# Performance work log

Hardware: AMD Instinct MI355X
Metric: run time of the kernel (lower is better)

Reference implementation:

```python
import jax, jax.numpy as jnp
import numpy as np

RES = 512
NUM_COMP = 64
INIT_SCALE = 0.1
N_PTS = 1048576


def setup_inputs() -> dict:
    key = jax.random.key(0)
    k1, k2 = jax.random.split(key)
    # points in [-1, 1] as the module expects
    in_tensor = jax.random.uniform(k1, (N_PTS, 3), dtype=jnp.float32, minval=-1.0, maxval=1.0)
    plane_coef = INIT_SCALE * jax.random.normal(k2, (3, NUM_COMP, RES, RES), dtype=jnp.float32)
    return {"in_tensor": in_tensor, "plane_coef": plane_coef}


def _sample_plane(coef, xy):
    """Bilinear grid_sample, align_corners=True, padding_mode='border'.

    coef: (C, R, R) feature plane; xy: (N, 2) coords in [-1, 1], xy[:,0]->W, xy[:,1]->H.
    Returns (C, N).
    """
    C, R, _ = coef.shape
    # unnormalize (align_corners=True), then border-clamp the coordinate itself
    fx = jnp.clip((xy[:, 0] + 1.0) * 0.5 * (R - 1), 0.0, R - 1)
    fy = jnp.clip((xy[:, 1] + 1.0) * 0.5 * (R - 1), 0.0, R - 1)
    x0 = jnp.floor(fx)
    y0 = jnp.floor(fy)
    wx = fx - x0
    wy = fy - y0
    x0i = x0.astype(jnp.int32)
    y0i = y0.astype(jnp.int32)
    x1i = jnp.minimum(x0i + 1, R - 1)
    y1i = jnp.minimum(y0i + 1, R - 1)
    flat = coef.reshape(C, R * R)  # gather via flat indices: idx = y*R + x

    def g(yi, xi):
        return flat[:, yi * R + xi]  # (C, N)

    return (g(y0i, x0i) * ((1.0 - wx) * (1.0 - wy))
            + g(y0i, x1i) * (wx * (1.0 - wy))
            + g(y1i, x0i) * ((1.0 - wx) * wy)
            + g(y1i, x1i) * (wx * wy))


def reference(in_tensor, plane_coef):
    orig_shape = in_tensor.shape
    pts = in_tensor.reshape(-1, 3)
    # projections onto the xy, xz, yz planes, matching torch order
    coords = jnp.stack([pts[:, jnp.array([0, 1])],
                        pts[:, jnp.array([0, 2])],
                        pts[:, jnp.array([1, 2])]], axis=0)  # (3, N, 2)
    feats = jax.vmap(_sample_plane)(plane_coef, coords)  # (3, C, N)
    out = feats.sum(0).T  # mode == 'sum' -> (N, C)
    return out.reshape(*orig_shape[:-1], -1)
```

## Files before the change

### kernel.cpp

```cpp
#include <hip/hip_runtime.h>

#define RES   512
#define NCH   64
#define SP    (RES * RES)

#define NBITS 5
#define NSIDE (1 << NBITS)
#define NBINS (1 << (3 * NBITS))

#define TRBLK 6144

typedef float     v4f __attribute__((ext_vector_type(4)));
typedef _Float16  h4  __attribute__((ext_vector_type(4)));

__device__ __forceinline__ v4f nt_load4(const float* p)
{
    return __builtin_nontemporal_load((const v4f*)p);
}
__device__ __forceinline__ void nt_store4(float* p, v4f v)
{
    __builtin_nontemporal_store(v, (v4f*)p);
}

__device__ __forceinline__ unsigned part1by2(unsigned v)
{
    v &= 0x3FF;
    v = (v | (v << 16)) & 0x030000FF;
    v = (v | (v <<  8)) & 0x0300F00F;
    v = (v | (v <<  4)) & 0x030C30C3;
    v = (v | (v <<  2)) & 0x09249249;
    return v;
}

__device__ __forceinline__ unsigned bin_of(float x, float y, float z)
{
    int ix = (int)((x + 1.0f) * 0.5f * (float)NSIDE);
    int iy = (int)((y + 1.0f) * 0.5f * (float)NSIDE);
    int iz = (int)((z + 1.0f) * 0.5f * (float)NSIDE);
    ix = min(max(ix, 0), NSIDE - 1);
    iy = min(max(iy, 0), NSIDE - 1);
    iz = min(max(iz, 0), NSIDE - 1);
    return part1by2((unsigned)ix) | (part1by2((unsigned)iy) << 1)
         | (part1by2((unsigned)iz) << 2);
}

__global__ __launch_bounds__(256) void transpose_hist(
    const float* __restrict__ in, _Float16* __restrict__ out,
    const float* __restrict__ pts, unsigned* __restrict__ hist, int npts)
{
    __shared__ float tile[64][129];

    int b = blockIdx.x;
    if (b >= TRBLK) {
        int i = (b - TRBLK) * 256 + threadIdx.x;
        if (i < npts) {
            float x = pts[3 * (size_t)i + 0];
            float y = pts[3 * (size_t)i + 1];
            float z = pts[3 * (size_t)i + 2];
            atomicAdd(&hist[bin_of(x, y, z)], 1u);
        }
        return;
    }

    int plane = b >> 11;
    int s0    = (b & 2047) << 7;
    const float* src = in  + (size_t)plane * NCH * SP;
    _Float16*    dst = out + (size_t)plane * SP  * NCH;

    int tid = threadIdx.x;
    int r   = tid >> 4;
    int c4  = (tid & 15) << 2;

    v4f vv[8];
    #pragma unroll
    for (int it = 0; it < 8; ++it) {
        int ch = r + (it & 3) * 16;
        int sp = ((it >> 2) << 6) + c4;
        vv[it] = nt_load4(src + (size_t)ch * SP + s0 + sp);
    }
    #pragma unroll
    for (int it = 0; it < 8; ++it) {
        int ch = r + (it & 3) * 16;
        int sp = ((it >> 2) << 6) + c4;
        tile[ch][sp + 0] = vv[it][0];
        tile[ch][sp + 1] = vv[it][1];
        tile[ch][sp + 2] = vv[it][2];
        tile[ch][sp + 3] = vv[it][3];
    }
    __syncthreads();
    #pragma unroll
    for (int it = 0; it < 8; ++it) {
        int s = r + (it & 3) * 16 + ((it >> 2) << 6);
        h4 v;
        v[0] = (_Float16)tile[c4 + 0][s];
        v[1] = (_Float16)tile[c4 + 1][s];
        v[2] = (_Float16)tile[c4 + 2][s];
        v[3] = (_Float16)tile[c4 + 3][s];
        *(h4*)(dst + (size_t)(s0 + s) * NCH + c4) = v;
    }
}

__global__ __launch_bounds__(1024) void scan_kernel(
    const unsigned* __restrict__ hist, unsigned* __restrict__ offs)
{
    __shared__ unsigned partial[1024];
    int t = threadIdx.x;
    unsigned base = (unsigned)t * 32;
    unsigned local[32];
    unsigned s = 0;
    #pragma unroll
    for (int k = 0; k < 32; ++k) { local[k] = s; s += hist[base + k]; }
    partial[t] = s;
    __syncthreads();
    for (int d = 1; d < 1024; d <<= 1) {
        unsigned v = (t >= d) ? partial[t - d] : 0u;
        __syncthreads();
        partial[t] += v;
        __syncthreads();
    }
    unsigned chunk_excl = (t == 0) ? 0u : partial[t - 1];
    #pragma unroll
    for (int k = 0; k < 32; ++k) offs[base + k] = chunk_excl + local[k];
}

__global__ __launch_bounds__(256) void scatter_kernel(
    const float* __restrict__ pts, unsigned* __restrict__ offs,
    float* __restrict__ spts4, int npts)
{
    int i = blockIdx.x * 256 + threadIdx.x;
    if (i >= npts) return;
    float x = pts[3 * (size_t)i + 0];
    float y = pts[3 * (size_t)i + 1];
    float z = pts[3 * (size_t)i + 2];
    unsigned pos = atomicAdd(&offs[bin_of(x, y, z)], 1u);
    v4f v;
    v[0] = x; v[1] = y; v[2] = z; v[3] = __uint_as_float((unsigned)i);
    *(v4f*)(spts4 + 4 * (size_t)pos) = v;
}

__global__ __launch_bounds__(256) void gather_sorted(
    const float* __restrict__ spts4,
    const _Float16* __restrict__ tp, float* __restrict__ out,
    int npts, int nblk)
{
    int cpx = nblk >> 3;
    int b   = blockIdx.x;
    int swz = (b & 7) * cpx + (b >> 3);
    int t   = swz * 256 + threadIdx.x;
    int j   = t >> 4;
    if (j >= npts) return;
    int cg  = (t & 15) << 2;

    v4f s = nt_load4(spts4 + 4 * (size_t)j);
    float px = s[0], py = s[1], pz = s[2];
    unsigned idx = __float_as_uint(s[3]);

    float us[3] = {px, px, py};
    float vs[3] = {py, pz, pz};

    v4f acc = {0.f, 0.f, 0.f, 0.f};

    #pragma unroll
    for (int pl = 0; pl < 3; ++pl) {
        float fx = fminf(fmaxf((us[pl] + 1.0f) * 0.5f * 511.0f, 0.0f), 511.0f);
        float fy = fminf(fmaxf((vs[pl] + 1.0f) * 0.5f * 511.0f, 0.0f), 511.0f);
        float x0f = floorf(fx), y0f = floorf(fy);
        int   x0  = (int)x0f,  y0  = (int)y0f;
        float wx  = fx - x0f,  wy  = fy - y0f;
        int   x1  = min(x0 + 1, RES - 1);
        int   y1  = min(y0 + 1, RES - 1);

        const _Float16* base = tp + (size_t)pl * SP * NCH;
        h4 a00 = *(const h4*)(base + ((size_t)(y0 * RES + x0) * NCH) + cg);
        h4 a01 = *(const h4*)(base + ((size_t)(y0 * RES + x1) * NCH) + cg);
        h4 a10 = *(const h4*)(base + ((size_t)(y1 * RES + x0) * NCH) + cg);
        h4 a11 = *(const h4*)(base + ((size_t)(y1 * RES + x1) * NCH) + cg);

        float w00 = (1.0f - wx) * (1.0f - wy);
        float w01 = wx * (1.0f - wy);
        float w10 = (1.0f - wx) * wy;
        float w11 = wx * wy;

        v4f v00 = {(float)a00[0], (float)a00[1], (float)a00[2], (float)a00[3]};
        v4f v01 = {(float)a01[0], (float)a01[1], (float)a01[2], (float)a01[3]};
        v4f v10 = {(float)a10[0], (float)a10[1], (float)a10[2], (float)a10[3]};
        v4f v11 = {(float)a11[0], (float)a11[1], (float)a11[2], (float)a11[3]};

        acc += w00 * v00 + w01 * v01 + w10 * v10 + w11 * v11;
    }

    nt_store4(out + (size_t)idx * NCH + cg, acc);
}

__global__ __launch_bounds__(256) void gather_tp(
    const float* __restrict__ pts,
    const _Float16* __restrict__ tp,
    float* __restrict__ out, int npts)
{
    int t  = blockIdx.x * 256 + threadIdx.x;
    int pt = t >> 4;
    if (pt >= npts) return;
    int cg = (t & 15) << 2;

    float px = pts[3 * (size_t)pt + 0];
    float py = pts[3 * (size_t)pt + 1];
    float pz = pts[3 * (size_t)pt + 2];

    float us[3] = {px, px, py};
    float vs[3] = {py, pz, pz};

    v4f acc = {0.f, 0.f, 0.f, 0.f};

    #pragma unroll
    for (int pl = 0; pl < 3; ++pl) {
        float fx = fminf(fmaxf((us[pl] + 1.0f) * 0.5f * 511.0f, 0.0f), 511.0f);
        float fy = fminf(fmaxf((vs[pl] + 1.0f) * 0.5f * 511.0f, 0.0f), 511.0f);
        float x0f = floorf(fx), y0f = floorf(fy);
        int   x0  = (int)x0f,  y0  = (int)y0f;
        float wx  = fx - x0f,  wy  = fy - y0f;
        int   x1  = min(x0 + 1, RES - 1);
        int   y1  = min(y0 + 1, RES - 1);

        const _Float16* base = tp + (size_t)pl * SP * NCH;
        h4 a00 = *(const h4*)(base + ((size_t)(y0 * RES + x0) * NCH) + cg);
        h4 a01 = *(const h4*)(base + ((size_t)(y0 * RES + x1) * NCH) + cg);
        h4 a10 = *(const h4*)(base + ((size_t)(y1 * RES + x0) * NCH) + cg);
        h4 a11 = *(const h4*)(base + ((size_t)(y1 * RES + x1) * NCH) + cg);

        float w00 = (1.0f - wx) * (1.0f - wy);
        float w01 = wx * (1.0f - wy);
        float w10 = (1.0f - wx) * wy;
        float w11 = wx * wy;

        v4f v00 = {(float)a00[0], (float)a00[1], (float)a00[2], (float)a00[3]};
        v4f v01 = {(float)a01[0], (float)a01[1], (float)a01[2], (float)a01[3]};
        v4f v10 = {(float)a10[0], (float)a10[1], (float)a10[2], (float)a10[3]};
        v4f v11 = {(float)a11[0], (float)a11[1], (float)a11[2], (float)a11[3]};

        acc += w00 * v00 + w01 * v01 + w10 * v10 + w11 * v11;
    }

    *(v4f*)(out + (size_t)pt * NCH + cg) = acc;
}

__global__ __launch_bounds__(256) void gather_direct(
    const float* __restrict__ pts,
    const float* __restrict__ planes,
    float* __restrict__ out, int npts)
{
    long t = (long)blockIdx.x * 256 + threadIdx.x;
    int pt = (int)(t >> 6);
    if (pt >= npts) return;
    int ch = (int)(t & 63);

    float px = pts[3 * (size_t)pt + 0];
    float py = pts[3 * (size_t)pt + 1];
    float pz = pts[3 * (size_t)pt + 2];
    float us[3] = {px, px, py};
    float vs[3] = {py, pz, pz};

    float acc = 0.0f;
    #pragma unroll
    for (int pl = 0; pl < 3; ++pl) {
        float fx = fminf(fmaxf((us[pl] + 1.0f) * 0.5f * 511.0f, 0.0f), 511.0f);
        float fy = fminf(fmaxf((vs[pl] + 1.0f) * 0.5f * 511.0f, 0.0f), 511.0f);
        float x0f = floorf(fx), y0f = floorf(fy);
        int   x0  = (int)x0f,  y0  = (int)y0f;
        float wx  = fx - x0f,  wy  = fy - y0f;
        int   x1  = min(x0 + 1, RES - 1);
        int   y1  = min(y0 + 1, RES - 1);

        const float* base = planes + (size_t)pl * NCH * SP + (size_t)ch * SP;
        float v00 = base[y0 * RES + x0];
        float v01 = base[y0 * RES + x1];
        float v10 = base[y1 * RES + x0];
        float v11 = base[y1 * RES + x1];

        acc += v00 * ((1.0f - wx) * (1.0f - wy))
             + v01 * (wx * (1.0f - wy))
             + v10 * ((1.0f - wx) * wy)
             + v11 * (wx * wy);
    }
    out[(size_t)pt * NCH + ch] = acc;
}

extern "C" void kernel_launch(void* const* d_in, const int* in_sizes, int n_in,
                              void* d_out, int out_size, void* d_ws, size_t ws_size,
                              hipStream_t stream)
{
    (void)n_in; (void)out_size;
    const float* pts    = (const float*)d_in[0];
    const float* planes = (const float*)d_in[1];
    float*       out    = (float*)d_out;
    int npts = in_sizes[0] / 3;

    size_t sz_tp     = (size_t)3 * NCH * SP * sizeof(_Float16);
    size_t off_spts  = sz_tp;
    size_t sz_spts   = (size_t)npts * 4 * sizeof(float);
    size_t off_hist  = off_spts + sz_spts;
    size_t off_offs  = off_hist + (size_t)NBINS * sizeof(unsigned);
    size_t need_sort = off_offs + (size_t)NBINS * sizeof(unsigned);

    int nptblk = (npts + 255) / 256;

    if (ws_size >= need_sort) {
        _Float16* tp   = (_Float16*)d_ws;
        float*    sp4  = (float*)((char*)d_ws + off_spts);
        unsigned* hist = (unsigned*)((char*)d_ws + off_hist);
        unsigned* offs = (unsigned*)((char*)d_ws + off_offs);

        hipMemsetAsync(hist, 0, (size_t)NBINS * sizeof(unsigned), stream);
        transpose_hist<<<TRBLK + nptblk, 256, 0, stream>>>(
            planes, tp, pts, hist, npts);
        scan_kernel<<<1, 1024, 0, stream>>>(hist, offs);
        scatter_kernel<<<nptblk, 256, 0, stream>>>(pts, offs, sp4, npts);

        long nthr = (long)npts * 16;
        int  nblk = (int)((nthr + 255) / 256);
        nblk = (nblk + 7) & ~7;
        gather_sorted<<<nblk, 256, 0, stream>>>(sp4, tp, out, npts, nblk);
    } else if (ws_size >= sz_tp) {
        transpose_hist<<<TRBLK, 256, 0, stream>>>(
            planes, (_Float16*)d_ws, nullptr, nullptr, 0);
        long nthr = (long)npts * 16;
        gather_tp<<<(int)((nthr + 255) / 256), 256, 0, stream>>>(
            pts, (const _Float16*)d_ws, out, npts);
    } else {
        long nthr = (long)npts * 64;
        gather_direct<<<(int)((nthr + 255) / 256), 256, 0, stream>>>(
            pts, planes, out, npts);
    }
}
```

Baseline: 609.1 us.

## Fuse plane transpose with point scatter and widen gather to 8 channels

```diff
diff --git a/kernel.cpp b/kernel.cpp
--- a/kernel.cpp
+++ b/kernel.cpp
@@ -8,10 +8,11 @@
 #define NSIDE (1 << NBITS)
 #define NBINS (1 << (3 * NBITS))
 
-#define TRBLK 6144
+#define TRBLK 3072
 
 typedef float     v4f __attribute__((ext_vector_type(4)));
 typedef _Float16  h4  __attribute__((ext_vector_type(4)));
+typedef _Float16  h8  __attribute__((ext_vector_type(8)));
 
 __device__ __forceinline__ v4f nt_load4(const float* p)
 {
@@ -44,60 +45,15 @@
          | (part1by2((unsigned)iz) << 2);
 }
 
-__global__ __launch_bounds__(256) void transpose_hist(
-    const float* __restrict__ in, _Float16* __restrict__ out,
+__global__ __launch_bounds__(256) void hist_kernel(
     const float* __restrict__ pts, unsigned* __restrict__ hist, int npts)
 {
-    __shared__ float tile[64][129];
-
-    int b = blockIdx.x;
-    if (b >= TRBLK) {
-        int i = (b - TRBLK) * 256 + threadIdx.x;
-        if (i < npts) {
-            float x = pts[3 * (size_t)i + 0];
-            float y = pts[3 * (size_t)i + 1];
-            float z = pts[3 * (size_t)i + 2];
-            atomicAdd(&hist[bin_of(x, y, z)], 1u);
-        }
-        return;
-    }
-
-    int plane = b >> 11;
-    int s0    = (b & 2047) << 7;
-    const float* src = in  + (size_t)plane * NCH * SP;
-    _Float16*    dst = out + (size_t)plane * SP  * NCH;
-
-    int tid = threadIdx.x;
-    int r   = tid >> 4;
-    int c4  = (tid & 15) << 2;
-
-    v4f vv[8];
-    #pragma unroll
-    for (int it = 0; it < 8; ++it) {
-        int ch = r + (it & 3) * 16;
-        int sp = ((it >> 2) << 6) + c4;
-        vv[it] = nt_load4(src + (size_t)ch * SP + s0 + sp);
-    }
-    #pragma unroll
-    for (int it = 0; it < 8; ++it) {
-        int ch = r + (it & 3) * 16;
-        int sp = ((it >> 2) << 6) + c4;
-        tile[ch][sp + 0] = vv[it][0];
-        tile[ch][sp + 1] = vv[it][1];
-        tile[ch][sp + 2] = vv[it][2];
-        tile[ch][sp + 3] = vv[it][3];
-    }
-    __syncthreads();
-    #pragma unroll
-    for (int it = 0; it < 8; ++it) {
-        int s = r + (it & 3) * 16 + ((it >> 2) << 6);
-        h4 v;
-        v[0] = (_Float16)tile[c4 + 0][s];
-        v[1] = (_Float16)tile[c4 + 1][s];
-        v[2] = (_Float16)tile[c4 + 2][s];
-        v[3] = (_Float16)tile[c4 + 3][s];
-        *(h4*)(dst + (size_t)(s0 + s) * NCH + c4) = v;
-    }
+    int i = blockIdx.x * 256 + threadIdx.x;
+    if (i >= npts) return;
+    float x = pts[3 * (size_t)i + 0];
+    float y = pts[3 * (size_t)i + 1];
+    float z = pts[3 * (size_t)i + 2];
+    atomicAdd(&hist[bin_of(x, y, z)], 1u);
 }
 
 __global__ __launch_bounds__(1024) void scan_kernel(
@@ -123,19 +79,65 @@
     for (int k = 0; k < 32; ++k) offs[base + k] = chunk_excl + local[k];
 }
 
-__global__ __launch_bounds__(256) void scatter_kernel(
+__global__ __launch_bounds__(256) void transpose_scatter(
+    const float* __restrict__ in, _Float16* __restrict__ outp,
     const float* __restrict__ pts, unsigned* __restrict__ offs,
     float* __restrict__ spts4, int npts)
 {
-    int i = blockIdx.x * 256 + threadIdx.x;
-    if (i >= npts) return;
-    float x = pts[3 * (size_t)i + 0];
-    float y = pts[3 * (size_t)i + 1];
-    float z = pts[3 * (size_t)i + 2];
-    unsigned pos = atomicAdd(&offs[bin_of(x, y, z)], 1u);
-    v4f v;
-    v[0] = x; v[1] = y; v[2] = z; v[3] = __uint_as_float((unsigned)i);
-    *(v4f*)(spts4 + 4 * (size_t)pos) = v;
+    __shared__ _Float16 tile[256][72];
+
+    int b    = blockIdx.x;
+    int id   = b >> 1;
+    if ((b & 1) == 0) {
+        if (pts == nullptr) return;
+        int i = id * 256 + threadIdx.x;
+        if (i < npts) {
+            float x = pts[3 * (size_t)i + 0];
+            float y = pts[3 * (size_t)i + 1];
+            float z = pts[3 * (size_t)i + 2];
+            unsigned pos = atomicAdd(&offs[bin_of(x, y, z)], 1u);
+            v4f v;
+            v[0] = x; v[1] = y; v[2] = z; v[3] = __uint_as_float((unsigned)i);
+            *(v4f*)(spts4 + 4 * (size_t)pos) = v;
+        }
+        return;
+    }
+    if (id >= TRBLK) return;
+
+    int plane = id >> 10;
+    int s0    = (id & 1023) << 8;
+    const float* src = in   + (size_t)plane * NCH * SP;
+    _Float16*    dst = outp + (size_t)plane * SP  * NCH;
+
+    int w = threadIdx.x >> 6;
+    int l = threadIdx.x & 63;
+
+    #pragma unroll
+    for (int g = 0; g < 4; ++g) {
+        int c0 = w * 16 + g * 4;
+        v4f v0 = nt_load4(src + (size_t)(c0 + 0) * SP + s0 + 4 * l);
+        v4f v1 = nt_load4(src + (size_t)(c0 + 1) * SP + s0 + 4 * l);
+        v4f v2 = nt_load4(src + (size_t)(c0 + 2) * SP + s0 + 4 * l);
+        v4f v3 = nt_load4(src + (size_t)(c0 + 3) * SP + s0 + 4 * l);
+        #pragma unroll
+        for (int i = 0; i < 4; ++i) {
+            h4 hv;
+            hv[0] = (_Float16)v0[i];
+            hv[1] = (_Float16)v1[i];
+            hv[2] = (_Float16)v2[i];
+            hv[3] = (_Float16)v3[i];
+            *(h4*)&tile[4 * l + i][c0] = hv;
+        }
+    }
+    __syncthreads();
+
+    #pragma unroll
+    for (int j = 0; j < 8; ++j) {
+        int texel = w * 64 + j * 8 + (l >> 3);
+        int oct   = (l & 7) << 3;
+        h8 hv = *(const h8*)&tile[texel][oct];
+        *(h8*)(dst + (size_t)(s0 + texel) * NCH + oct) = hv;
+    }
 }
 
 __global__ __launch_bounds__(256) void gather_sorted(
@@ -147,9 +149,9 @@
     int b   = blockIdx.x;
     int swz = (b & 7) * cpx + (b >> 3);
     int t   = swz * 256 + threadIdx.x;
-    int j   = t >> 4;
+    int j   = t >> 3;
     if (j >= npts) return;
-    int cg  = (t & 15) << 2;
+    int cg  = (t & 7) << 3;
 
     v4f s = nt_load4(spts4 + 4 * (size_t)j);
     float px = s[0], py = s[1], pz = s[2];
@@ -158,7 +160,8 @@
     float us[3] = {px, px, py};
     float vs[3] = {py, pz, pz};
 
-    v4f acc = {0.f, 0.f, 0.f, 0.f};
+    v4f acc0 = {0.f, 0.f, 0.f, 0.f};
+    v4f acc1 = {0.f, 0.f, 0.f, 0.f};
 
     #pragma unroll
     for (int pl = 0; pl < 3; ++pl) {
@@ -171,25 +174,27 @@
         int   y1  = min(y0 + 1, RES - 1);
 
         const _Float16* base = tp + (size_t)pl * SP * NCH;
-        h4 a00 = *(const h4*)(base + ((size_t)(y0 * RES + x0) * NCH) + cg);
-        h4 a01 = *(const h4*)(base + ((size_t)(y0 * RES + x1) * NCH) + cg);
-        h4 a10 = *(const h4*)(base + ((size_t)(y1 * RES + x0) * NCH) + cg);
-        h4 a11 = *(const h4*)(base + ((size_t)(y1 * RES + x1) * NCH) + cg);
+        h8 a00 = *(const h8*)(base + ((size_t)(y0 * RES + x0) * NCH) + cg);
+        h8 a01 = *(const h8*)(base + ((size_t)(y0 * RES + x1) * NCH) + cg);
+        h8 a10 = *(const h8*)(base + ((size_t)(y1 * RES + x0) * NCH) + cg);
+        h8 a11 = *(const h8*)(base + ((size_t)(y1 * RES + x1) * NCH) + cg);
 
         float w00 = (1.0f - wx) * (1.0f - wy);
         float w01 = wx * (1.0f - wy);
         float w10 = (1.0f - wx) * wy;
         float w11 = wx * wy;
 
-        v4f v00 = {(float)a00[0], (float)a00[1], (float)a00[2], (float)a00[3]};
-        v4f v01 = {(float)a01[0], (float)a01[1], (float)a01[2], (float)a01[3]};
-        v4f v10 = {(float)a10[0], (float)a10[1], (float)a10[2], (float)a10[3]};
-        v4f v11 = {(float)a11[0], (float)a11[1], (float)a11[2], (float)a11[3]};
-
-        acc += w00 * v00 + w01 * v01 + w10 * v10 + w11 * v11;
-    }
-
-    nt_store4(out + (size_t)idx * NCH + cg, acc);
+        #pragma unroll
+        for (int k = 0; k < 4; ++k) {
+            acc0[k] += w00 * (float)a00[k] + w01 * (float)a01[k]
+                     + w10 * (float)a10[k] + w11 * (float)a11[k];
+            acc1[k] += w00 * (float)a00[k + 4] + w01 * (float)a01[k + 4]
+                     + w10 * (float)a10[k + 4] + w11 * (float)a11[k + 4];
+        }
+    }
+
+    nt_store4(out + (size_t)idx * NCH + cg,     acc0);
+    nt_store4(out + (size_t)idx * NCH + cg + 4, acc1);
 }
 
 __global__ __launch_bounds__(256) void gather_tp(
@@ -198,9 +203,9 @@
     float* __restrict__ out, int npts)
 {
     int t  = blockIdx.x * 256 + threadIdx.x;
-    int pt = t >> 4;
+    int pt = t >> 3;
     if (pt >= npts) return;
-    int cg = (t & 15) << 2;
+    int cg = (t & 7) << 3;
 
     float px = pts[3 * (size_t)pt + 0];
     float py = pts[3 * (size_t)pt + 1];
@@ -209,7 +214,8 @@
     float us[3] = {px, px, py};
     float vs[3] = {py, pz, pz};
 
-    v4f acc = {0.f, 0.f, 0.f, 0.f};
+    v4f acc0 = {0.f, 0.f, 0.f, 0.f};
+    v4f acc1 = {0.f, 0.f, 0.f, 0.f};
 
     #pragma unroll
     for (int pl = 0; pl < 3; ++pl) {
@@ -222,25 +228,27 @@
         int   y1  = min(y0 + 1, RES - 1);
 
         const _Float16* base = tp + (size_t)pl * SP * NCH;
-        h4 a00 = *(const h4*)(base + ((size_t)(y0 * RES + x0) * NCH) + cg);
-        h4 a01 = *(const h4*)(base + ((size_t)(y0 * RES + x1) * NCH) + cg);
-        h4 a10 = *(const h4*)(base + ((size_t)(y1 * RES + x0) * NCH) + cg);
-        h4 a11 = *(const h4*)(base + ((size_t)(y1 * RES + x1) * NCH) + cg);
+        h8 a00 = *(const h8*)(base + ((size_t)(y0 * RES + x0) * NCH) + cg);
+        h8 a01 = *(const h8*)(base + ((size_t)(y0 * RES + x1) * NCH) + cg);
+        h8 a10 = *(const h8*)(base + ((size_t)(y1 * RES + x0) * NCH) + cg);
+        h8 a11 = *(const h8*)(base + ((size_t)(y1 * RES + x1) * NCH) + cg);
 
         float w00 = (1.0f - wx) * (1.0f - wy);
         float w01 = wx * (1.0f - wy);
         float w10 = (1.0f - wx) * wy;
         float w11 = wx * wy;
 
-        v4f v00 = {(float)a00[0], (float)a00[1], (float)a00[2], (float)a00[3]};
-        v4f v01 = {(float)a01[0], (float)a01[1], (float)a01[2], (float)a01[3]};
-        v4f v10 = {(float)a10[0], (float)a10[1], (float)a10[2], (float)a10[3]};
-        v4f v11 = {(float)a11[0], (float)a11[1], (float)a11[2], (float)a11[3]};
-
-        acc += w00 * v00 + w01 * v01 + w10 * v10 + w11 * v11;
-    }
-
-    *(v4f*)(out + (size_t)pt * NCH + cg) = acc;
+        #pragma unroll
+        for (int k = 0; k < 4; ++k) {
+            acc0[k] += w00 * (float)a00[k] + w01 * (float)a01[k]
+                     + w10 * (float)a10[k] + w11 * (float)a11[k];
+            acc1[k] += w00 * (float)a00[k + 4] + w01 * (float)a01[k + 4]
+                     + w10 * (float)a10[k + 4] + w11 * (float)a11[k + 4];
+        }
+    }
+
+    *(v4f*)(out + (size_t)pt * NCH + cg)     = acc0;
+    *(v4f*)(out + (size_t)pt * NCH + cg + 4) = acc1;
 }
 
 __global__ __launch_bounds__(256) void gather_direct(
@@ -310,19 +318,21 @@
         unsigned* offs = (unsigned*)((char*)d_ws + off_offs);
 
         hipMemsetAsync(hist, 0, (size_t)NBINS * sizeof(unsigned), stream);
-        transpose_hist<<<TRBLK + nptblk, 256, 0, stream>>>(
-            planes, tp, pts, hist, npts);
+        hist_kernel<<<nptblk, 256, 0, stream>>>(pts, hist, npts);
         scan_kernel<<<1, 1024, 0, stream>>>(hist, offs);
-        scatter_kernel<<<nptblk, 256, 0, stream>>>(pts, offs, sp4, npts);
-
-        long nthr = (long)npts * 16;
+
+        int half = (nptblk > TRBLK) ? nptblk : TRBLK;
+        transpose_scatter<<<2 * half, 256, 0, stream>>>(
+            planes, tp, pts, offs, sp4, npts);
+
+        long nthr = (long)npts * 8;
         int  nblk = (int)((nthr + 255) / 256);
         nblk = (nblk + 7) & ~7;
         gather_sorted<<<nblk, 256, 0, stream>>>(sp4, tp, out, npts, nblk);
     } else if (ws_size >= sz_tp) {
-        transpose_hist<<<TRBLK, 256, 0, stream>>>(
-            planes, (_Float16*)d_ws, nullptr, nullptr, 0);
-        long nthr = (long)npts * 16;
+        transpose_scatter<<<2 * TRBLK, 256, 0, stream>>>(
+            planes, (_Float16*)d_ws, nullptr, nullptr, nullptr, 0);
+        long nthr = (long)npts * 8;
         gather_tp<<<(int)((nthr + 255) / 256), 256, 0, stream>>>(
             pts, (const _Float16*)d_ws, out, npts);
     } else {
```

After: 550.8 us. 9.6% less time.
